# Performance work log

Measured on AMD Instinct MI355X. Metric: run time of the kernel, lower is better.

## Reference

```python
import jax, jax.numpy as jnp
import numpy as np
import math

N = 10000      # atoms
E = 320000     # neighbor pairs (edges)
NELEM = 3      # species one-hot size
NRAD = 8       # radial channels per component
NB = 8         # bessel basis size
ZETA = 4       # max angular moment
RC = 5.0       # radial cutoff
S = 4          # species embedding size (species_layer_sizes[-1])
NCOMP = (ZETA + 2) * NRAD   # 2-body slice + (ZETA+1) angular slices = 48
FEAT = NCOMP * S            # 192

# multinomial expansion of (r_i . r_j)^l : lxlylz powers and l!/(lx!ly!lz!) norms
_TERMS = []
for l in range(ZETA + 1):
    pw, nm = [], []
    for a in range(l + 1):
        for b in range(l + 1 - a):
            c = l - a - b
            pw.append((a, b, c))
            nm.append(math.factorial(l) / (math.factorial(a) * math.factorial(b) * math.factorial(c)))
    _TERMS.append((np.array(pw, dtype=np.float32), np.array(nm, dtype=np.float32)))


def _silu(x):
    return x * jax.nn.sigmoid(x)


def setup_inputs() -> dict:
    key = jax.random.key(0)
    ks = jax.random.split(key, 12)
    rij = (jax.random.uniform(ks[0], (E, 3), minval=-1.0, maxval=1.0) * (RC / math.sqrt(3.0))).astype(jnp.float32)
    first_atom = jax.random.randint(ks[1], (E,), 0, N, dtype=jnp.int32)
    second_atom = jax.random.randint(ks[2], (E,), 0, N, dtype=jnp.int32)
    species_idx = jax.random.randint(ks[3], (N,), 0, NELEM, dtype=jnp.int32)
    w = lambda k, s: (jax.random.normal(k, s) * 0.1).astype(jnp.float32)
    z = lambda s: jnp.zeros(s, jnp.float32)
    return dict(
        rij=rij, species_idx=species_idx, first_atom=first_atom, second_atom=second_atom,
        Wr1=w(ks[4], (NB, 64)), br1=z((64,)),
        Wr2=w(ks[5], (64, NCOMP)), br2=z((NCOMP,)),
        Ws1=w(ks[6], (NELEM, 16)), bs1=z((16,)),
        Ws2=w(ks[7], (16, S)), bs2=z((S,)),
        Wa1=w(ks[8], (FEAT, 64)), ba1=z((64,)),
        Wa2=w(ks[9], (64, 64)), ba2=z((64,)),
        Wa3=w(ks[10], (64, 1)), ba3=z((1,)),
    )


def reference(rij, species_idx, first_atom, second_atom,
              Wr1, br1, Wr2, br2, Ws1, bs1, Ws2, bs2,
              Wa1, ba1, Wa2, ba2, Wa3, ba3):
    d = jnp.sqrt(jnp.sum(rij * rij, axis=-1) + 1e-12)            # [E]
    rhat = rij / d[:, None]                                       # [E,3]
    fc = jnp.where(d < RC, 0.5 * (jnp.cos(np.pi * d / RC) + 1.0), 0.0)
    n = jnp.arange(1, NB + 1, dtype=rij.dtype)
    bes = jnp.sqrt(2.0 / RC) * jnp.sin(n[None, :] * np.pi * d[:, None] / RC) / d[:, None]  # [E,NB]
    # learned radial functions, all components at once, smoothed by cutoff
    R = _silu(_silu(bes @ Wr1 + br1) @ Wr2 + br2) * fc[:, None]   # [E, NCOMP]
    # species encoder -> per-atom embedding, gathered on neighbor atom j
    onehot = jax.nn.one_hot(species_idx, NELEM, dtype=rij.dtype)  # [N,NELEM]
    semb = jnp.tanh(onehot @ Ws1 + bs1) @ Ws2 + bs2               # [N,S]
    sj = semb[second_atom]                                        # [E,S]
    # 2-body feature
    feats = [jax.ops.segment_sum(R[:, :NRAD, None] * sj[:, None, :], first_atom, num_segments=N)]  # [N,NRAD,S]
    off = NRAD
    for l in range(ZETA + 1):
        pw, nm = _TERMS[l]
        comps = jnp.prod(rhat[:, None, :] ** jnp.asarray(pw)[None, :, :], axis=-1)  # [E,C_l]
        Rl = R[:, off:off + NRAD]
        off += NRAD
        edge = Rl[:, :, None, None] * comps[:, None, :, None] * sj[:, None, None, :]  # [E,NRAD,C_l,S]
        A = jax.ops.segment_sum(edge, first_atom, num_segments=N)                     # [N,NRAD,C_l,S]
        feats.append(jnp.einsum('nrcs,c->nrs', A * A, jnp.asarray(nm)))               # [N,NRAD,S]
    feat = jnp.concatenate(feats, axis=1).reshape(N, -1)          # [N, FEAT]
    h = _silu(feat @ Wa1 + ba1)
    h = _silu(h @ Wa2 + ba2)
    return (h @ Wa3 + ba3)[:, 0]                                  # per-atom energies [N]
```

## Files before the change

kernel.cpp:

```cpp
#include <hip/hip_runtime.h>
#include <math.h>

#define NATOMS 10000
#define NEDGES 320000
#define NBINS  (NATOMS * 4)
#define RC_F 5.0f
#define PI_F 3.14159265358979323846f

#define NK   4096
#define TROW 48
#define HINV_F ((float)(NK - 1) / RC_F)

#define WS_SEMB   0
#define WS_GTOT   12
#define WS_CNT    16
#define WS_OFFS   40016
#define WS_CURSOR 80016
#define WS_EIDX   120016
#define WS_TAB    440096

__device__ __constant__ int   d_PWA[35] = {0, 0,0,1, 0,0,0,1,1,2, 0,0,0,0,1,1,1,2,2,3, 0,0,0,0,0,1,1,1,1,2,2,2,3,3,4};
__device__ __constant__ int   d_PWB[35] = {0, 0,1,0, 0,1,2,0,1,0, 0,1,2,3,0,1,2,0,1,0, 0,1,2,3,4,0,1,2,3,0,1,2,0,1,0};
__device__ __constant__ int   d_PWC[35] = {0, 1,0,0, 2,1,0,1,0,0, 3,2,1,0,2,1,0,1,0,0, 4,3,2,1,0,3,2,1,0,2,1,0,1,0,0};
__device__ __constant__ float d_NM[35]  = {1.f, 1.f,1.f,1.f, 1.f,2.f,1.f,2.f,2.f,1.f,
                                           1.f,3.f,3.f,1.f,3.f,6.f,3.f,3.f,3.f,1.f,
                                           1.f,4.f,6.f,4.f,1.f,4.f,12.f,12.f,4.f,6.f,12.f,6.f,4.f,4.f,1.f};
__device__ __constant__ int   d_LBLK[35]= {0, 1,1,1, 2,2,2,2,2,2, 3,3,3,3,3,3,3,3,3,3, 4,4,4,4,4,4,4,4,4,4,4,4,4,4,4};
__device__ __constant__ int   d_L6[6]   = {0,1,4,10,20,35};

__device__ __forceinline__ float siluf(float x) { return x / (1.0f + __expf(-x)); }

__device__ __forceinline__ float2 f2fma(float2 a, float2 b, float2 c) {
  return make_float2(fmaf(a.x, b.x, c.x), fmaf(a.y, b.y, c.y));
}

__device__ __forceinline__ float psel(float x, int p) {
  float x2 = x * x;
  float r = 1.0f;
  r = (p == 1) ? x : r;
  r = (p == 2) ? x2 : r;
  r = (p == 3) ? x2 * x : r;
  r = (p == 4) ? x2 * x2 : r;
  return r;
}

__global__ void k_init(const float* __restrict__ Ws1, const float* __restrict__ bs1,
                       const float* __restrict__ Ws2, const float* __restrict__ bs2,
                       float* __restrict__ ws)
{
  int tid = blockIdx.x * blockDim.x + threadIdx.x;
  int* cnt = (int*)(ws + WS_CNT);
  if (tid < NBINS) cnt[tid] = 0;
  if (tid == 0) *(int*)(ws + WS_GTOT) = 0;
  if (tid < 12) {
    int t = tid >> 2, s = tid & 3;
    float acc = bs2[s];
    for (int j = 0; j < 16; j++) acc += tanhf(Ws1[t * 16 + j] + bs1[j]) * Ws2[j * 4 + s];
    ws[WS_SEMB + tid] = acc;
  }
}

__global__ __launch_bounds__(192) void k_table(
    const float* __restrict__ Wr1, const float* __restrict__ br1,
    const float* __restrict__ Wr2, const float* __restrict__ br2,
    float* __restrict__ ws)
{
  int sl = threadIdx.x;
  int k  = blockIdx.x * 16 + threadIdx.y;
  float dk = (float)k * (RC_F / (float)(NK - 1));
  float d = fmaxf(dk, 1e-6f);
  float invd = 1.0f / d;

  float theta = (PI_F / RC_F) * d;
  float s1 = sinf(theta), c1 = cosf(theta);
  float fc = (d < RC_F) ? 0.5f * (c1 + 1.0f) : 0.0f;
  float bes[8];
  {
    float sq = sqrtf(2.0f / RC_F) * invd;
    float twoc = 2.0f * c1;
    float sp = 0.0f, sc = s1;
    #pragma unroll
    for (int q = 0; q < 8; q++) {
      bes[q] = sq * sc;
      float sn = twoc * sc - sp;
      sp = sc; sc = sn;
    }
  }

  float h1[64];
  #pragma unroll
  for (int j4 = 0; j4 < 16; j4++) {
    float2 a01 = *(const float2*)&br1[j4 * 4];
    float2 a23 = *(const float2*)&br1[j4 * 4 + 2];
    #pragma unroll
    for (int q = 0; q < 8; q++) {
      float2 b2 = make_float2(bes[q], bes[q]);
      a01 = f2fma(b2, *(const float2*)&Wr1[q * 64 + j4 * 4],     a01);
      a23 = f2fma(b2, *(const float2*)&Wr1[q * 64 + j4 * 4 + 2], a23);
    }
    h1[j4 * 4 + 0] = siluf(a01.x);
    h1[j4 * 4 + 1] = siluf(a01.y);
    h1[j4 * 4 + 2] = siluf(a23.x);
    h1[j4 * 4 + 3] = siluf(a23.y);
  }

  int j0 = sl * 4;
  float2 a01 = *(const float2*)&br2[j0];
  float2 a23 = *(const float2*)&br2[j0 + 2];
  for (int q = 0; q < 64; q++) {
    float2 h2 = make_float2(h1[q], h1[q]);
    a01 = f2fma(h2, *(const float2*)&Wr2[q * 48 + j0],     a01);
    a23 = f2fma(h2, *(const float2*)&Wr2[q * 48 + j0 + 2], a23);
  }
  *(float4*)(ws + WS_TAB + (size_t)k * TROW + j0) =
      make_float4(siluf(a01.x) * fc, siluf(a01.y) * fc,
                  siluf(a23.x) * fc, siluf(a23.y) * fc);
}

__global__ void k_hist(const int* __restrict__ first_atom, const int* __restrict__ second_atom,
                       const int* __restrict__ species, float* __restrict__ ws)
{
  int e = blockIdx.x * blockDim.x + threadIdx.x;
  if (e < NEDGES) {
    int* cnt = (int*)(ws + WS_CNT);
    int bin = first_atom[e] * 4 + species[second_atom[e]];
    atomicAdd(&cnt[bin], 1);
  }
}

__global__ __launch_bounds__(256) void k_alloc(float* __restrict__ ws)
{
  const int4* cnt4 = (const int4*)(ws + WS_CNT);
  int4* offs4   = (int4*)(ws + WS_OFFS);
  int4* cursor4 = (int4*)(ws + WS_CURSOR);
  int* gtot = (int*)(ws + WS_GTOT);
  __shared__ int wsum[4];
  __shared__ int sbase;
  int tid = threadIdx.x;
  int lane = tid & 63, wv = tid >> 6;
  int a = blockIdx.x * 256 + tid;
  bool live = (a < NATOMS);
  int4 c = live ? cnt4[a] : make_int4(0, 0, 0, 0);
  int s = c.x + c.y + c.z + c.w;
  int inc = s;
  #pragma unroll
  for (int d = 1; d < 64; d <<= 1) {
    int v = __shfl_up(inc, d, 64);
    if (lane >= d) inc += v;
  }
  if (lane == 63) wsum[wv] = inc;
  __syncthreads();
  if (tid == 0) sbase = atomicAdd(gtot, wsum[0] + wsum[1] + wsum[2] + wsum[3]);
  __syncthreads();
  int woff = sbase;
  for (int w = 0; w < wv; w++) woff += wsum[w];
  int o0 = woff + inc - s;
  if (live) {
    int4 o;
    o.x = o0;
    o.y = o.x + c.x;
    o.z = o.y + c.y;
    o.w = o.z + c.z;
    offs4[a] = o;
    cursor4[a] = o;
  }
}

__global__ __launch_bounds__(256) void k_scatter(
    const int* __restrict__ first_atom, const int* __restrict__ second_atom,
    const int* __restrict__ species, float* __restrict__ ws)
{
  int e = blockIdx.x * 256 + threadIdx.x;
  int* cursor = (int*)(ws + WS_CURSOR);
  int* eidx   = (int*)(ws + WS_EIDX);
  int a = first_atom[e];
  int t = species[second_atom[e]];
  int pos = atomicAdd(&cursor[a * 4 + t], 1);
  eidx[pos] = e;
}

__global__ __launch_bounds__(128) void k_atom(
    const float* __restrict__ ws, const float* __restrict__ rijg,
    const float* __restrict__ Wa1, const float* __restrict__ ba1,
    const float* __restrict__ Wa2, const float* __restrict__ ba2,
    const float* __restrict__ Wa3, const float* __restrict__ ba3,
    float* __restrict__ out)
{
  __shared__ __align__(16) float sScr[2][2784];
  int tid = threadIdx.x;
  int lane = tid & 63, wv = tid >> 6;
  int a = blockIdx.x * 2 + wv;
  float* sStage = &sScr[wv][0];
  float* sG     = &sScr[wv][1664];
  float* sFeat  = &sScr[wv][2528];
  float* sH     = &sScr[wv][2720];

  const int* eidx = (const int*)(ws + WS_EIDX);
  const float* tab = ws + WS_TAB;
  int4 o = ((const int4*)(ws + WS_OFFS))[a];

  const int c = lane;
  bool isc = (c < 35);
  int pa = 0, pb = 0, pcw = 0, lb = 0;
  if (isc) { pa = d_PWA[c]; pb = d_PWB[c]; pcw = d_PWC[c]; lb = d_LBLK[c]; }
  int rdir = lane - 35;
  bool isd = (rdir >= 0) && (rdir < 8);
  int rl = lane >> 4, fl = lane & 15;

  float2 g2[3][4];
  #pragma unroll
  for (int t2 = 0; t2 < 3; t2++)
    #pragma unroll
    for (int r = 0; r < 4; r++) g2[t2][r] = make_float2(0.f, 0.f);
  float g0[3] = {0.0f, 0.0f, 0.0f};

#define CORE(T) {                                                             \
    const float* rb = sStage + j * 52;                                        \
    if (isc) {                                                                \
      float comp = psel(rb[48], pa) * psel(rb[49], pb) * psel(rb[50], pcw);   \
      float2 c2v = make_float2(comp, comp);                                   \
      const float2* r2 = (const float2*)(rb + 8 + 8 * lb);                    \
      g2[T][0] = f2fma(c2v, r2[0], g2[T][0]);                                 \
      g2[T][1] = f2fma(c2v, r2[1], g2[T][1]);                                 \
      g2[T][2] = f2fma(c2v, r2[2], g2[T][2]);                                 \
      g2[T][3] = f2fma(c2v, r2[3], g2[T][3]);                                 \
    } else if (isd) {                                                         \
      g0[T] += rb[rdir];                                                      \
    }                                                                         \
  }

#define RUN(T, LO, HI)                                                        \
  for (int cb = (LO); cb < (HI); cb += 32) {                                  \
    int m = (HI) - cb; if (m > 32) m = 32;                                    \
    int pp = cb + lane;                                                       \
    int e = eidx[(lane < m) ? pp : cb];                                       \
    float x = rijg[e * 3 + 0], y = rijg[e * 3 + 1], z = rijg[e * 3 + 2];      \
    float dd = sqrtf(x * x + y * y + z * z + 1e-12f);                         \
    float invd = 1.0f / dd;                                                   \
    float rx = x * invd, ry = y * invd, rz = z * invd;                        \
    float fi = dd * HINV_F;                                                   \
    int ii = (int)fi;                                                         \
    ii = (ii < 1) ? 1 : ((ii > NK - 3) ? NK - 3 : ii);                        \
    float w = fi - (float)ii;                                                 \
    float wm = w - 1.0f, wp = w + 1.0f, w2c = w - 2.0f;                       \
    float l0 = -w * wm * w2c * (1.0f / 6.0f);                                 \
    float l1 = wp * wm * w2c * 0.5f;                                          \
    float l2 = -wp * w * w2c * 0.5f;                                          \
    float l3 = wp * w * wm * (1.0f / 6.0f);                                   \
    int rowb = (ii - 1) * TROW;                                               \
    int R = (m + 3) >> 2;                                                     \
    for (int r = 0; r < R; r++) {                                             \
      int sl = r * 4 + rl;                                                    \
      float b0 = __shfl(l0, sl, 64), b1 = __shfl(l1, sl, 64);                 \
      float b2 = __shfl(l2, sl, 64), b3 = __shfl(l3, sl, 64);                 \
      int   rbI = __shfl(rowb, sl, 64);                                       \
      float sx = __shfl(rx, sl, 64), sy = __shfl(ry, sl, 64);                 \
      float sz = __shfl(rz, sl, 64);                                          \
      if (fl < 12) {                                                          \
        const float* tp = tab + rbI + fl * 4;                                 \
        float4 t0 = *(const float4*)(tp);                                     \
        float4 t1 = *(const float4*)(tp + TROW);                              \
        float4 t2 = *(const float4*)(tp + 2 * TROW);                          \
        float4 t3 = *(const float4*)(tp + 3 * TROW);                          \
        float4 v;                                                             \
        v.x = fmaf(b3, t3.x, fmaf(b2, t2.x, fmaf(b1, t1.x, b0 * t0.x)));      \
        v.y = fmaf(b3, t3.y, fmaf(b2, t2.y, fmaf(b1, t1.y, b0 * t0.y)));      \
        v.z = fmaf(b3, t3.z, fmaf(b2, t2.z, fmaf(b1, t1.z, b0 * t0.z)));      \
        v.w = fmaf(b3, t3.w, fmaf(b2, t2.w, fmaf(b1, t1.w, b0 * t0.w)));      \
        *(float4*)(sStage + sl * 52 + fl * 4) = v;                            \
      } else if (fl == 12) {                                                  \
        *(float4*)(sStage + sl * 52 + 48) = make_float4(sx, sy, sz, 0.0f);    \
      }                                                                       \
    }                                                                         \
    for (int j = 0; j < m; j++) CORE(T)                                       \
  }

  RUN(0, o.x, o.y)
  RUN(1, o.y, o.z)
  RUN(2, o.z, o.w)
#undef RUN
#undef CORE

  if (isc) {
    #pragma unroll
    for (int t2 = 0; t2 < 3; t2++)
      #pragma unroll
      for (int r = 0; r < 8; r++) {
        float gval = (r & 1) ? g2[t2][r >> 1].y : g2[t2][r >> 1].x;
        sG[(t2 * 8 + r) * 36 + c] = gval;
      }
  } else if (isd) {
    #pragma unroll
    for (int t2 = 0; t2 < 3; t2++) sG[(t2 * 8 + rdir) * 36 + 35] = g0[t2];
  }

  int s = lane & 3;
  float se0 = ws[WS_SEMB + s], se1 = ws[WS_SEMB + 4 + s], se2 = ws[WS_SEMB + 8 + s];
  float fout[3];
  #pragma unroll
  for (int u = 0; u < 3; u++) {
    int f = lane + 64 * u;
    int blk = f >> 5, rr = (f >> 2) & 7;
    float acc;
    if (blk == 0) {
      acc = se0 * sG[(0 + rr) * 36 + 35] + se1 * sG[(8 + rr) * 36 + 35] + se2 * sG[(16 + rr) * 36 + 35];
    } else {
      int c0 = d_L6[blk - 1], c1 = d_L6[blk];
      acc = 0.0f;
      for (int cc = c0; cc < c1; cc++) {
        float A = se0 * sG[(0 + rr) * 36 + cc] + se1 * sG[(8 + rr) * 36 + cc] + se2 * sG[(16 + rr) * 36 + cc];
        acc += d_NM[cc] * A * A;
      }
    }
    fout[u] = acc;
  }
  #pragma unroll
  for (int u = 0; u < 3; u++) sFeat[lane + 64 * u] = fout[u];

  {
    float a0 = 0.f, a1 = 0.f, a2 = 0.f, a3 = 0.f;
    for (int k4 = 0; k4 < 48; k4++) {
      float4 f4 = *(const float4*)(sFeat + k4 * 4);
      const float* wp = Wa1 + (k4 * 4) * 64 + lane;
      a0 += f4.x * wp[0];
      a1 += f4.y * wp[64];
      a2 += f4.z * wp[128];
      a3 += f4.w * wp[192];
    }
    sH[lane] = siluf(a0 + a1 + a2 + a3 + ba1[lane]);
  }

  {
    float a0 = 0.f, a1 = 0.f, a2 = 0.f, a3 = 0.f;
    for (int k4 = 0; k4 < 16; k4++) {
      float4 h4 = *(const float4*)(sH + k4 * 4);
      const float* wp = Wa2 + (k4 * 4) * 64 + lane;
      a0 += h4.x * wp[0];
      a1 += h4.y * wp[64];
      a2 += h4.z * wp[128];
      a3 += h4.w * wp[192];
    }
    float h2 = siluf(a0 + a1 + a2 + a3 + ba2[lane]);
    float pr = h2 * Wa3[lane];
    #pragma unroll
    for (int off = 32; off > 0; off >>= 1) pr += __shfl_down(pr, off, 64);
    if (lane == 0) out[a] = pr + ba3[0];
  }
}

extern "C" void kernel_launch(void* const* d_in, const int* in_sizes, int n_in,
                              void* d_out, int out_size, void* d_ws, size_t ws_size,
                              hipStream_t stream)
{
  const float* rij         = (const float*)d_in[0];
  const int*   species     = (const int*)  d_in[1];
  const int*   first_atom  = (const int*)  d_in[2];
  const int*   second_atom = (const int*)  d_in[3];
  const float* Wr1 = (const float*)d_in[4];
  const float* br1 = (const float*)d_in[5];
  const float* Wr2 = (const float*)d_in[6];
  const float* br2 = (const float*)d_in[7];
  const float* Ws1 = (const float*)d_in[8];
  const float* bs1 = (const float*)d_in[9];
  const float* Ws2 = (const float*)d_in[10];
  const float* bs2 = (const float*)d_in[11];
  const float* Wa1 = (const float*)d_in[12];
  const float* ba1 = (const float*)d_in[13];
  const float* Wa2 = (const float*)d_in[14];
  const float* ba2 = (const float*)d_in[15];
  const float* Wa3 = (const float*)d_in[16];
  const float* ba3 = (const float*)d_in[17];
  float* ws  = (float*)d_ws;
  float* out = (float*)d_out;

  k_init<<<(NBINS + 255) / 256, 256, 0, stream>>>(Ws1, bs1, Ws2, bs2, ws);
  k_table<<<NK / 16, dim3(12, 16), 0, stream>>>(Wr1, br1, Wr2, br2, ws);
  k_hist<<<(NEDGES + 255) / 256, 256, 0, stream>>>(first_atom, second_atom, species, ws);
  k_alloc<<<(NATOMS + 255) / 256, 256, 0, stream>>>(ws);
  k_scatter<<<NEDGES / 256, 256, 0, stream>>>(first_atom, second_atom, species, ws);
  k_atom<<<NATOMS / 2, 128, 0, stream>>>(ws, rij, Wa1, ba1, Wa2, ba2, Wa3, ba3, out);
}
```

Baseline: 205.8 us.

## Pre-sort edge geometry, switch to linear table interpolation, fuse init into table

```diff
diff --git a/kernel.cpp b/kernel.cpp
--- a/kernel.cpp
+++ b/kernel.cpp
@@ -7,7 +7,7 @@
 #define RC_F 5.0f
 #define PI_F 3.14159265358979323846f
 
-#define NK   4096
+#define NK   16384
 #define TROW 48
 #define HINV_F ((float)(NK - 1) / RC_F)
 
@@ -16,8 +16,9 @@
 #define WS_CNT    16
 #define WS_OFFS   40016
 #define WS_CURSOR 80016
-#define WS_EIDX   120016
-#define WS_TAB    440096
+#define WS_BIN    120016
+#define WS_SD     440096
+#define WS_TAB    1720096
 
 __device__ __constant__ int   d_PWA[35] = {0, 0,0,1, 0,0,0,1,1,2, 0,0,0,0,1,1,1,2,2,3, 0,0,0,0,0,1,1,1,1,2,2,2,3,3,4};
 __device__ __constant__ int   d_PWB[35] = {0, 0,1,0, 0,1,2,0,1,0, 0,1,2,3,0,1,2,0,1,0, 0,1,2,3,4,0,1,2,3,0,1,2,0,1,0};
@@ -44,27 +45,24 @@
   return r;
 }
 
-__global__ void k_init(const float* __restrict__ Ws1, const float* __restrict__ bs1,
-                       const float* __restrict__ Ws2, const float* __restrict__ bs2,
-                       float* __restrict__ ws)
-{
-  int tid = blockIdx.x * blockDim.x + threadIdx.x;
-  int* cnt = (int*)(ws + WS_CNT);
-  if (tid < NBINS) cnt[tid] = 0;
-  if (tid == 0) *(int*)(ws + WS_GTOT) = 0;
-  if (tid < 12) {
-    int t = tid >> 2, s = tid & 3;
-    float acc = bs2[s];
-    for (int j = 0; j < 16; j++) acc += tanhf(Ws1[t * 16 + j] + bs1[j]) * Ws2[j * 4 + s];
-    ws[WS_SEMB + tid] = acc;
-  }
-}
-
 __global__ __launch_bounds__(192) void k_table(
     const float* __restrict__ Wr1, const float* __restrict__ br1,
     const float* __restrict__ Wr2, const float* __restrict__ br2,
+    const float* __restrict__ Ws1, const float* __restrict__ bs1,
+    const float* __restrict__ Ws2, const float* __restrict__ bs2,
     float* __restrict__ ws)
 {
+  int flat = blockIdx.x * 192 + threadIdx.y * 12 + threadIdx.x;
+  int* cnt = (int*)(ws + WS_CNT);
+  if (flat < NBINS) cnt[flat] = 0;
+  if (flat == 0) *(int*)(ws + WS_GTOT) = 0;
+  if (flat < 12) {
+    int t = flat >> 2, s = flat & 3;
+    float acc = bs2[s];
+    for (int j = 0; j < 16; j++) acc += tanhf(Ws1[t * 16 + j] + bs1[j]) * Ws2[j * 4 + s];
+    ws[WS_SEMB + flat] = acc;
+  }
+
   int sl = threadIdx.x;
   int k  = blockIdx.x * 16 + threadIdx.y;
   float dk = (float)k * (RC_F / (float)(NK - 1));
@@ -117,15 +115,16 @@
                   siluf(a23.x) * fc, siluf(a23.y) * fc);
 }
 
-__global__ void k_hist(const int* __restrict__ first_atom, const int* __restrict__ second_atom,
-                       const int* __restrict__ species, float* __restrict__ ws)
-{
-  int e = blockIdx.x * blockDim.x + threadIdx.x;
-  if (e < NEDGES) {
-    int* cnt = (int*)(ws + WS_CNT);
-    int bin = first_atom[e] * 4 + species[second_atom[e]];
-    atomicAdd(&cnt[bin], 1);
-  }
+__global__ __launch_bounds__(256) void k_hist(
+    const int* __restrict__ first_atom, const int* __restrict__ second_atom,
+    const int* __restrict__ species, float* __restrict__ ws)
+{
+  int e = blockIdx.x * 256 + threadIdx.x;
+  int* cnt  = (int*)(ws + WS_CNT);
+  int* binA = (int*)(ws + WS_BIN);
+  int bin = first_atom[e] * 4 + species[second_atom[e]];
+  atomicAdd(&cnt[bin], 1);
+  binA[e] = bin;
 }
 
 __global__ __launch_bounds__(256) void k_alloc(float* __restrict__ ws)
@@ -167,35 +166,36 @@
 }
 
 __global__ __launch_bounds__(256) void k_scatter(
-    const int* __restrict__ first_atom, const int* __restrict__ second_atom,
-    const int* __restrict__ species, float* __restrict__ ws)
+    const float* __restrict__ rij, float* __restrict__ ws)
 {
   int e = blockIdx.x * 256 + threadIdx.x;
   int* cursor = (int*)(ws + WS_CURSOR);
-  int* eidx   = (int*)(ws + WS_EIDX);
-  int a = first_atom[e];
-  int t = species[second_atom[e]];
-  int pos = atomicAdd(&cursor[a * 4 + t], 1);
-  eidx[pos] = e;
+  const int* binA = (const int*)(ws + WS_BIN);
+  int bin = binA[e];
+  int pos = atomicAdd(&cursor[bin], 1);
+  float x = rij[e * 3 + 0], y = rij[e * 3 + 1], z = rij[e * 3 + 2];
+  float d = sqrtf(x * x + y * y + z * z + 1e-12f);
+  float invd = 1.0f / d;
+  ((float4*)(ws + WS_SD))[pos] = make_float4(x * invd, y * invd, z * invd, d);
 }
 
 __global__ __launch_bounds__(128) void k_atom(
-    const float* __restrict__ ws, const float* __restrict__ rijg,
+    const float* __restrict__ ws,
     const float* __restrict__ Wa1, const float* __restrict__ ba1,
     const float* __restrict__ Wa2, const float* __restrict__ ba2,
     const float* __restrict__ Wa3, const float* __restrict__ ba3,
     float* __restrict__ out)
 {
-  __shared__ __align__(16) float sScr[2][2784];
+  __shared__ __align__(16) float sScr[2][1120];
   int tid = threadIdx.x;
   int lane = tid & 63, wv = tid >> 6;
   int a = blockIdx.x * 2 + wv;
   float* sStage = &sScr[wv][0];
-  float* sG     = &sScr[wv][1664];
-  float* sFeat  = &sScr[wv][2528];
-  float* sH     = &sScr[wv][2720];
-
-  const int* eidx = (const int*)(ws + WS_EIDX);
+  float* sG     = &sScr[wv][0];
+  float* sFeat  = &sScr[wv][864];
+  float* sH     = &sScr[wv][1056];
+
+  const float4* sd4 = (const float4*)(ws + WS_SD);
   const float* tab = ws + WS_TAB;
   int4 o = ((const int4*)(ws + WS_OFFS))[a];
 
@@ -217,7 +217,8 @@
 #define CORE(T) {                                                             \
     const float* rb = sStage + j * 52;                                        \
     if (isc) {                                                                \
-      float comp = psel(rb[48], pa) * psel(rb[49], pb) * psel(rb[50], pcw);   \
+      float4 rh = *(const float4*)(rb + 48);                                  \
+      float comp = psel(rh.x, pa) * psel(rh.y, pb) * psel(rh.z, pcw);         \
       float2 c2v = make_float2(comp, comp);                                   \
       const float2* r2 = (const float2*)(rb + 8 + 8 * lb);                    \
       g2[T][0] = f2fma(c2v, r2[0], g2[T][0]);                                 \
@@ -230,43 +231,31 @@
   }
 
 #define RUN(T, LO, HI)                                                        \
-  for (int cb = (LO); cb < (HI); cb += 32) {                                  \
-    int m = (HI) - cb; if (m > 32) m = 32;                                    \
+  for (int cb = (LO); cb < (HI); cb += 16) {                                  \
+    int m = (HI) - cb; if (m > 16) m = 16;                                    \
     int pp = cb + lane;                                                       \
-    int e = eidx[(lane < m) ? pp : cb];                                       \
-    float x = rijg[e * 3 + 0], y = rijg[e * 3 + 1], z = rijg[e * 3 + 2];      \
-    float dd = sqrtf(x * x + y * y + z * z + 1e-12f);                         \
-    float invd = 1.0f / dd;                                                   \
-    float rx = x * invd, ry = y * invd, rz = z * invd;                        \
-    float fi = dd * HINV_F;                                                   \
+    float4 ed = sd4[(lane < m) ? pp : (HI - 1)];                              \
+    float fi = ed.w * HINV_F;                                                 \
     int ii = (int)fi;                                                         \
-    ii = (ii < 1) ? 1 : ((ii > NK - 3) ? NK - 3 : ii);                        \
+    ii = (ii > NK - 2) ? (NK - 2) : ii;                                       \
     float w = fi - (float)ii;                                                 \
-    float wm = w - 1.0f, wp = w + 1.0f, w2c = w - 2.0f;                       \
-    float l0 = -w * wm * w2c * (1.0f / 6.0f);                                 \
-    float l1 = wp * wm * w2c * 0.5f;                                          \
-    float l2 = -wp * w * w2c * 0.5f;                                          \
-    float l3 = wp * w * wm * (1.0f / 6.0f);                                   \
-    int rowb = (ii - 1) * TROW;                                               \
+    int rowb = ii * TROW;                                                     \
     int R = (m + 3) >> 2;                                                     \
     for (int r = 0; r < R; r++) {                                             \
       int sl = r * 4 + rl;                                                    \
-      float b0 = __shfl(l0, sl, 64), b1 = __shfl(l1, sl, 64);                 \
-      float b2 = __shfl(l2, sl, 64), b3 = __shfl(l3, sl, 64);                 \
-      int   rbI = __shfl(rowb, sl, 64);                                       \
-      float sx = __shfl(rx, sl, 64), sy = __shfl(ry, sl, 64);                 \
-      float sz = __shfl(rz, sl, 64);                                          \
+      float w_s = __shfl(w, sl, 64);                                          \
+      int   rb_ = __shfl(rowb, sl, 64);                                       \
+      float sx = __shfl(ed.x, sl, 64), sy = __shfl(ed.y, sl, 64);             \
+      float sz = __shfl(ed.z, sl, 64);                                        \
       if (fl < 12) {                                                          \
-        const float* tp = tab + rbI + fl * 4;                                 \
+        const float* tp = tab + rb_ + fl * 4;                                 \
         float4 t0 = *(const float4*)(tp);                                     \
         float4 t1 = *(const float4*)(tp + TROW);                              \
-        float4 t2 = *(const float4*)(tp + 2 * TROW);                          \
-        float4 t3 = *(const float4*)(tp + 3 * TROW);                          \
         float4 v;                                                             \
-        v.x = fmaf(b3, t3.x, fmaf(b2, t2.x, fmaf(b1, t1.x, b0 * t0.x)));      \
-        v.y = fmaf(b3, t3.y, fmaf(b2, t2.y, fmaf(b1, t1.y, b0 * t0.y)));      \
-        v.z = fmaf(b3, t3.z, fmaf(b2, t2.z, fmaf(b1, t1.z, b0 * t0.z)));      \
-        v.w = fmaf(b3, t3.w, fmaf(b2, t2.w, fmaf(b1, t1.w, b0 * t0.w)));      \
+        v.x = fmaf(w_s, t1.x - t0.x, t0.x);                                   \
+        v.y = fmaf(w_s, t1.y - t0.y, t0.y);                                   \
+        v.z = fmaf(w_s, t1.z - t0.z, t0.z);                                   \
+        v.w = fmaf(w_s, t1.w - t0.w, t0.w);                                   \
         *(float4*)(sStage + sl * 52 + fl * 4) = v;                            \
       } else if (fl == 12) {                                                  \
         *(float4*)(sStage + sl * 52 + 48) = make_float4(sx, sy, sz, 0.0f);    \
@@ -373,10 +362,9 @@
   float* ws  = (float*)d_ws;
   float* out = (float*)d_out;
 
-  k_init<<<(NBINS + 255) / 256, 256, 0, stream>>>(Ws1, bs1, Ws2, bs2, ws);
-  k_table<<<NK / 16, dim3(12, 16), 0, stream>>>(Wr1, br1, Wr2, br2, ws);
-  k_hist<<<(NEDGES + 255) / 256, 256, 0, stream>>>(first_atom, second_atom, species, ws);
+  k_table<<<NK / 16, dim3(12, 16), 0, stream>>>(Wr1, br1, Wr2, br2, Ws1, bs1, Ws2, bs2, ws);
+  k_hist<<<NEDGES / 256, 256, 0, stream>>>(first_atom, second_atom, species, ws);
   k_alloc<<<(NATOMS + 255) / 256, 256, 0, stream>>>(ws);
-  k_scatter<<<NEDGES / 256, 256, 0, stream>>>(first_atom, second_atom, species, ws);
-  k_atom<<<NATOMS / 2, 128, 0, stream>>>(ws, rij, Wa1, ba1, Wa2, ba2, Wa3, ba3, out);
-}
+  k_scatter<<<NEDGES / 256, 256, 0, stream>>>(rij, ws);
+  k_atom<<<NATOMS / 2, 128, 0, stream>>>(ws, Wa1, ba1, Wa2, ba2, Wa3, ba3, out);
+}
```

After: 186.8 us. -9.2%, faster.
